# Performance work log

Hardware: AMD Instinct MI355X
Metric: run time of the kernel (lower is better)

The kernel has to match this reference:

```python
import jax, jax.numpy as jnp
import numpy as np

N_NODES = 50000
N_EDGES = 800000
N_GRAPHS = 64
IN_CH = 128
HID_CH = 128
OUT_CH = 2


def setup_inputs() -> dict:
    key = jax.random.key(0)
    k = jax.random.split(key, 7)
    x = jax.random.normal(k[0], (N_NODES, IN_CH), dtype=jnp.float32)
    edge_index = jax.random.randint(k[1], (2, N_EDGES), 0, N_NODES, dtype=jnp.int64)
    batch = jnp.sort(jax.random.randint(k[2], (N_NODES,), 0, N_GRAPHS, dtype=jnp.int64))
    W1 = jax.random.normal(k[3], (IN_CH, HID_CH), dtype=jnp.float32) * 0.05
    b1 = jnp.zeros((HID_CH,), dtype=jnp.float32)
    W2 = jax.random.normal(k[4], (HID_CH, OUT_CH), dtype=jnp.float32) * 0.05
    b2 = jnp.zeros((OUT_CH,), dtype=jnp.float32)
    return {"x": x, "edge_index": edge_index, "batch": batch,
            "W1": W1, "b1": b1, "W2": W2, "b2": b2}


def gcn_conv(x, edge_index, W, b):
    """PyG GCNConv: add self-loops, symmetric D^{-1/2}(A+I)D^{-1/2} aggregation of XW, plus bias."""
    n = x.shape[0]
    loop = jnp.arange(n, dtype=edge_index.dtype)
    src = jnp.concatenate([edge_index[0], loop])  # [E+N]
    dst = jnp.concatenate([edge_index[1], loop])
    ones = jnp.ones_like(dst, dtype=x.dtype)
    deg = jax.ops.segment_sum(ones, dst, num_segments=n)      # in-degree incl. self-loop (>=1)
    d_inv_sqrt = jax.lax.rsqrt(deg)
    norm = d_inv_sqrt[src] * d_inv_sqrt[dst]                  # [E+N]
    h = x @ W                                                 # [N, out]
    msg = h[src] * norm[:, None]                              # gather + scale
    out = jax.ops.segment_sum(msg, dst, num_segments=n)       # scatter-add
    return out + b


def global_mean_pool(x, batch, num_graphs):
    sums = jax.ops.segment_sum(x, batch, num_segments=num_graphs)
    cnt = jax.ops.segment_sum(jnp.ones((x.shape[0],), dtype=x.dtype), batch, num_segments=num_graphs)
    return sums / jnp.maximum(cnt, 1.0)[:, None]


def reference(x, edge_index, batch, W1, b1, W2, b2):
    h = jax.nn.relu(gcn_conv(x, edge_index, W1, b1))
    h = gcn_conv(h, edge_index, W2, b2)
    out = global_mean_pool(h, batch, N_GRAPHS)  # [G, out_channels]
    # dropout in eval mode == identity
    return out
```

## Files before the change

kernel.cpp:

```cpp
#include <hip/hip_runtime.h>


#define NGRAPH 64
#define CH 128
#define BSUB 384
#define NCOPY 8
#define BCAPT (BSUB * NCOPY)
#define CSTR 4096

typedef float f32x4 __attribute__((ext_vector_type(4)));
typedef _Float16 f16x8 __attribute__((ext_vector_type(8)));
typedef _Float16 f16x4 __attribute__((ext_vector_type(4)));
typedef _Float16 f16x2 __attribute__((ext_vector_type(2)));

__global__ void k_init(int* __restrict__ bcur8, float* __restrict__ gsum,
                       int* __restrict__ gcnt, int* __restrict__ done,
                       float* __restrict__ h2,
                       const float* __restrict__ W1, _Float16* __restrict__ w1t,
                       int NB, int N) {
    int i = blockIdx.x * blockDim.x + threadIdx.x;
    if (i < NB * NCOPY) bcur8[i] = 0;
    if (i < 2 * NGRAPH) gsum[i] = 0.f;
    if (i < NGRAPH) gcnt[i] = 0;
    if (i == 0) *done = 0;
    if (i < 2) h2[2 * N + i] = 0.f;
    if (i < CH * CH) {
        int k = i >> 7, c = i & 127;
        w1t[c * CH + k] = (_Float16)W1[i];
    }
}

__global__ __launch_bounds__(256) void k_bin(const int* __restrict__ src,
                                             const int* __restrict__ dst,
                                             int* __restrict__ bcur8,
                                             unsigned int* __restrict__ tmp,
                                             int E, int EPB) {
    __shared__ int hist[512];
    __shared__ int gbase[512];
    __shared__ int cur[512];
    int t = threadIdx.x;
    int e0 = blockIdx.x * EPB;
    int e1 = min(E, e0 + EPB);
    for (int i = t; i < 512; i += 256) { hist[i] = 0; cur[i] = 0; }
    __syncthreads();
    for (int e = e0 + t; e < e1; e += 256)
        atomicAdd(&hist[dst[e] >> 7], 1);
    __syncthreads();
    int copy = blockIdx.x & (NCOPY - 1);
    for (int b = t; b < 512; b += 256) {
        int hc = hist[b];
        if (hc) gbase[b] = atomicAdd(&bcur8[b * NCOPY + copy], hc);
    }
    __syncthreads();
    for (int e = e0 + t; e < e1; e += 256) {
        int d = dst[e];
        int b = d >> 7;
        int li = atomicAdd(&cur[b], 1);
        int pos = gbase[b] + li;
        if (pos < BSUB)
            tmp[(size_t)b * BCAPT + copy * BSUB + pos] =
                ((unsigned)(d & 127) << 25) | (unsigned)src[e];
    }
}

__global__ __launch_bounds__(256) void k_build(const unsigned int* __restrict__ tmp,
                                               const int* __restrict__ bcur8,
                                               int2* __restrict__ rs2,
                                               float* __restrict__ dinv,
                                               int* __restrict__ csr, int N) {
    __shared__ int hist[128];
    __shared__ int scan[128];
    __shared__ int lcur[128];
    int b = blockIdx.x, t = threadIdx.x;
    if (t < 128) hist[t] = 0;
    __syncthreads();
    const unsigned int* tb = tmp + (size_t)b * BCAPT;
    for (int c = 0; c < NCOPY; c++) {
        int cnt = min(bcur8[b * NCOPY + c], BSUB);
        const unsigned int* tp = tb + c * BSUB;
        for (int e = t; e < cnt; e += 256) atomicAdd(&hist[tp[e] >> 25], 1);
    }
    __syncthreads();
    int val = 0, v = 0, pv = 0;
    if (t < 128) { v = hist[t]; pv = (v + 7) & ~7; val = pv; scan[t] = val; }
    __syncthreads();
    for (int off = 1; off < 128; off <<= 1) {
        int add = (t >= off && t < 128) ? scan[t - off] : 0;
        __syncthreads();
        if (t < 128) { val += add; scan[t] = val; }
        __syncthreads();
    }
    int base = b * CSTR;
    if (t < 128) {
        int excl = val - pv;
        lcur[t] = excl;
        int n = b * 128 + t;
        if (n < N) {
            rs2[n] = make_int2(base + excl, pv);
            dinv[n] = rsqrtf((float)(v + 1));
            for (int e = v; e < pv; e++) csr[base + excl + e] = N;
        }
    }
    __syncthreads();
    for (int c = 0; c < NCOPY; c++) {
        int cnt = min(bcur8[b * NCOPY + c], BSUB);
        const unsigned int* tp = tb + c * BSUB;
        for (int e = t; e < cnt; e += 256) {
            unsigned p = tp[e];
            int pos = atomicAdd(&lcur[p >> 25], 1);
            csr[base + pos] = (int)(p & 0x01FFFFFFu);
        }
    }
}

__global__ __launch_bounds__(256) void k_gemm1(const float* __restrict__ X,
                                               const _Float16* __restrict__ w1t,
                                               const float* __restrict__ dinv,
                                               _Float16* __restrict__ H, int N) {
    __shared__ _Float16 Xs[64 * 136];
    __shared__ _Float16 Ws[128 * 136];
    int t = threadIdx.x;
    int row0 = blockIdx.x * 64;
    const float4* Xv = (const float4*)X;

    #pragma unroll
    for (int i = 0; i < 8; i++) {
        int gi = t + i * 256;
        int r = gi >> 5, c4 = gi & 31;
        int gr = row0 + r;
        float4 v = (gr < N) ? Xv[(size_t)gr * 32 + c4] : make_float4(0.f, 0.f, 0.f, 0.f);
        f16x4 hv = {(_Float16)v.x, (_Float16)v.y, (_Float16)v.z, (_Float16)v.w};
        *(f16x4*)&Xs[r * 136 + 4 * c4] = hv;
    }
    #pragma unroll
    for (int i = 0; i < 8; i++) {
        int gi = t + i * 256;
        int r = gi >> 4, cc = gi & 15;
        f16x8 vv = *(const f16x8*)&w1t[r * CH + cc * 8];
        *(f16x8*)&Ws[r * 136 + cc * 8] = vv;
    }
    __syncthreads();

    int w = t >> 6, l = t & 63;
    int r0w = w * 16;
    int lr = l & 15, lk = (l >> 4) * 8;
    f32x4 acc[8] = {};
    #pragma unroll
    for (int k0 = 0; k0 < 128; k0 += 32) {
        f16x8 a = *(const f16x8*)&Xs[(r0w + lr) * 136 + k0 + lk];
        #pragma unroll
        for (int c = 0; c < 8; c++) {
            f16x8 bf = *(const f16x8*)&Ws[(c * 16 + lr) * 136 + k0 + lk];
            acc[c] = __builtin_amdgcn_mfma_f32_16x16x32_f16(a, bf, acc[c], 0, 0, 0);
        }
    }
    float dv[4];
    #pragma unroll
    for (int q = 0; q < 4; q++) {
        int gr = row0 + r0w + (l >> 4) * 4 + q;
        dv[q] = (gr < N) ? dinv[gr] : 0.f;
    }
    __syncthreads();
    #pragma unroll
    for (int c = 0; c < 8; c++)
        #pragma unroll
        for (int q = 0; q < 4; q++)
            Xs[(r0w + (l >> 4) * 4 + q) * 136 + c * 16 + lr] = (_Float16)(acc[c][q] * dv[q]);
    __syncthreads();
    f16x2* Hv = (f16x2*)H;
    #pragma unroll
    for (int i = 0; i < 16; i++) {
        int gi = t + i * 256;
        int r = gi >> 6, cp = gi & 63;
        int gr = row0 + r;
        Hv[(size_t)gr * 64 + cp] = *(f16x2*)&Xs[r * 136 + 2 * cp];
    }
}

__global__ __launch_bounds__(256) void k_layer1(const _Float16* __restrict__ h,
                                                const int* __restrict__ csr,
                                                const int2* __restrict__ rs2,
                                                const float* __restrict__ dinv,
                                                const float* __restrict__ b1,
                                                const float* __restrict__ W2,
                                                float* __restrict__ h2, int N) {
    int n = (blockIdx.x * 256 + threadIdx.x) >> 6;
    int l = threadIdx.x & 63;
    if (n >= N) return;
    const f16x2* hv = (const f16x2*)h;
    float dn = dinv[n];
    f16x2 self = hv[(size_t)n * 64 + l];
    float acc0 = (float)self.x, acc1 = (float)self.y;
    int2 rs = rs2[n];
    int base = rs.x, cnt = rs.y;
    for (int c0 = 0; c0 < cnt; c0 += 64) {
        int m = cnt - c0; if (m > 64) m = 64;
        int idx = csr[base + c0 + l];
        for (int j = 0; j < m; j += 8) {
            int s0 = __shfl(idx, j + 0), s1 = __shfl(idx, j + 1);
            int s2 = __shfl(idx, j + 2), s3 = __shfl(idx, j + 3);
            int s4 = __shfl(idx, j + 4), s5 = __shfl(idx, j + 5);
            int s6 = __shfl(idx, j + 6), s7 = __shfl(idx, j + 7);
            f16x2 v0 = hv[(size_t)s0 * 64 + l];
            f16x2 v1 = hv[(size_t)s1 * 64 + l];
            f16x2 v2 = hv[(size_t)s2 * 64 + l];
            f16x2 v3 = hv[(size_t)s3 * 64 + l];
            f16x2 v4 = hv[(size_t)s4 * 64 + l];
            f16x2 v5 = hv[(size_t)s5 * 64 + l];
            f16x2 v6 = hv[(size_t)s6 * 64 + l];
            f16x2 v7 = hv[(size_t)s7 * 64 + l];
            acc0 += (float)v0.x; acc1 += (float)v0.y;
            acc0 += (float)v1.x; acc1 += (float)v1.y;
            acc0 += (float)v2.x; acc1 += (float)v2.y;
            acc0 += (float)v3.x; acc1 += (float)v3.y;
            acc0 += (float)v4.x; acc1 += (float)v4.y;
            acc0 += (float)v5.x; acc1 += (float)v5.y;
            acc0 += (float)v6.x; acc1 += (float)v6.y;
            acc0 += (float)v7.x; acc1 += (float)v7.y;
        }
    }
    float2 bb = ((const float2*)b1)[l];
    float v0 = fmaxf(fmaf(dn, acc0, bb.x), 0.f);
    float v1 = fmaxf(fmaf(dn, acc1, bb.y), 0.f);
    float4 w2 = ((const float4*)W2)[l];
    float p0 = fmaf(v0, w2.x, v1 * w2.z);
    float p1 = fmaf(v0, w2.y, v1 * w2.w);
    #pragma unroll
    for (int off = 32; off; off >>= 1) {
        p0 += __shfl_xor(p0, off);
        p1 += __shfl_xor(p1, off);
    }
    if (l == 0) ((float2*)h2)[n] = make_float2(p0 * dn, p1 * dn);
}

__global__ __launch_bounds__(256) void k_layer2_pool(const float* __restrict__ h2,
                                                     const int* __restrict__ csr,
                                                     const int2* __restrict__ rs2,
                                                     const float* __restrict__ dinv,
                                                     const int* __restrict__ batch,
                                                     float* __restrict__ gsum,
                                                     int* __restrict__ gcnt,
                                                     int* __restrict__ done,
                                                     const float* __restrict__ b2,
                                                     float* __restrict__ out, int N) {
    __shared__ float ssum[2 * NGRAPH];
    __shared__ int scnt[NGRAPH];
    __shared__ int s_last;
    int t = threadIdx.x;
    if (t < 2 * NGRAPH) ssum[t] = 0.f;
    if (t < NGRAPH) scnt[t] = 0;
    __syncthreads();
    int n = blockIdx.x * blockDim.x + t;
    if (n < N) {
        const float2* h2v = (const float2*)h2;
        float dn = dinv[n];
        float2 a = h2v[n];
        int2 rs = rs2[n];
        for (int e = rs.x; e < rs.x + rs.y; e++) {
            float2 v = h2v[csr[e]];
            a.x += v.x;
            a.y += v.y;
        }
        a.x *= dn;
        a.y *= dn;
        int g = batch[n];
        atomicAdd(&ssum[g * 2 + 0], a.x);
        atomicAdd(&ssum[g * 2 + 1], a.y);
        atomicAdd(&scnt[g], 1);
    }
    __syncthreads();
    if (t < 2 * NGRAPH) atomicAdd(&gsum[t], ssum[t]);
    if (t < NGRAPH) atomicAdd(&gcnt[t], scnt[t]);
    __syncthreads();
    if (t == 0) {
        __threadfence();
        int r = atomicAdd(done, 1);
        s_last = (r == (int)gridDim.x - 1) ? 1 : 0;
    }
    __syncthreads();
    if (s_last && t < 2 * NGRAPH) {
        int g = t >> 1, c = t & 1;
        float sv = atomicAdd(&gsum[t], 0.f);
        float cv = (float)atomicAdd(&gcnt[g], 0);
        out[t] = sv / fmaxf(cv, 1.f) + b2[c];
    }
}

extern "C" void kernel_launch(void* const* d_in, const int* in_sizes, int n_in,
                              void* d_out, int out_size, void* d_ws, size_t ws_size,
                              hipStream_t stream) {
    const float* x     = (const float*)d_in[0];
    const int*   ei    = (const int*)d_in[1];
    const int*   batch = (const int*)d_in[2];
    const float* W1    = (const float*)d_in[3];
    const float* b1    = (const float*)d_in[4];
    const float* W2    = (const float*)d_in[5];
    const float* b2    = (const float*)d_in[6];
    float* out = (float*)d_out;

    int N = in_sizes[0] / CH;
    int E = in_sizes[1] / 2;
    int NB = (N + 127) / 128;
    const int* esrc = ei;
    const int* edst = ei + E;

    char* w = (char*)d_ws;
    auto alloc = [&](size_t bytes) -> void* {
        void* p = (void*)w;
        w += (bytes + 255) & ~(size_t)255;
        return p;
    };
    _Float16* h      = (_Float16*)alloc((size_t)(N + 64) * CH * sizeof(_Float16));
    float* dinv      = (float*)alloc((size_t)N * sizeof(float));
    int2* rs2        = (int2*) alloc((size_t)N * sizeof(int2));
    int* csr         = (int*)  alloc((size_t)NB * CSTR * sizeof(int));
    float* h2        = (float*)alloc((size_t)(N + 1) * 2 * sizeof(float));
    int* bcur8       = (int*)  alloc((size_t)NB * NCOPY * sizeof(int));
    _Float16* w1t    = (_Float16*)alloc((size_t)CH * CH * sizeof(_Float16));
    float* gsum      = (float*)alloc(128 * sizeof(float));
    int* gcnt        = (int*)  alloc(64 * sizeof(int));
    int* done        = (int*)  alloc(256);
    unsigned int* tmp = (unsigned int*)h;

    int nbN = (N + 255) / 256;
    int NCHUNK = 256;
    int EPB = (E + NCHUNK - 1) / NCHUNK;

    k_init  <<<64, 256, 0, stream>>>(bcur8, gsum, gcnt, done, h2, W1, w1t, NB, N);
    k_bin   <<<NCHUNK, 256, 0, stream>>>(esrc, edst, bcur8, tmp, E, EPB);
    k_build <<<NB, 256, 0, stream>>>(tmp, bcur8, rs2, dinv, csr, N);
    k_gemm1 <<<(N + 63) / 64, 256, 0, stream>>>(x, w1t, dinv, h, N);
    k_layer1<<<(N * 64 + 255) / 256, 256, 0, stream>>>(h, csr, rs2, dinv, b1, W2, h2, N);
    k_layer2_pool<<<nbN, 256, 0, stream>>>(h2, csr, rs2, dinv, batch, gsum, gcnt,
                                           done, b2, out, N);
}
```

Baseline: 169.7 us.

## Fold init into binning kernel, read W1 directly in GEMM, retune bin copies

```diff
diff --git a/kernel.cpp b/kernel.cpp
--- a/kernel.cpp
+++ b/kernel.cpp
@@ -3,71 +3,66 @@
 
 #define NGRAPH 64
 #define CH 128
-#define BSUB 384
-#define NCOPY 8
+#define NTHR 256
+#define NBIN 512
+#define NCOPY 16
+#define BSUB 224
 #define BCAPT (BSUB * NCOPY)
-#define CSTR 4096
+#define CSTR 4608
 
 typedef float f32x4 __attribute__((ext_vector_type(4)));
 typedef _Float16 f16x8 __attribute__((ext_vector_type(8)));
 typedef _Float16 f16x4 __attribute__((ext_vector_type(4)));
 typedef _Float16 f16x2 __attribute__((ext_vector_type(2)));
 
-__global__ void k_init(int* __restrict__ bcur8, float* __restrict__ gsum,
-                       int* __restrict__ gcnt, int* __restrict__ done,
-                       float* __restrict__ h2,
-                       const float* __restrict__ W1, _Float16* __restrict__ w1t,
-                       int NB, int N) {
-    int i = blockIdx.x * blockDim.x + threadIdx.x;
-    if (i < NB * NCOPY) bcur8[i] = 0;
-    if (i < 2 * NGRAPH) gsum[i] = 0.f;
-    if (i < NGRAPH) gcnt[i] = 0;
-    if (i == 0) *done = 0;
-    if (i < 2) h2[2 * N + i] = 0.f;
-    if (i < CH * CH) {
-        int k = i >> 7, c = i & 127;
-        w1t[c * CH + k] = (_Float16)W1[i];
-    }
-}
-
-__global__ __launch_bounds__(256) void k_bin(const int* __restrict__ src,
-                                             const int* __restrict__ dst,
-                                             int* __restrict__ bcur8,
-                                             unsigned int* __restrict__ tmp,
-                                             int E, int EPB) {
+__global__ __launch_bounds__(NTHR) void k_bin(const int* __restrict__ src,
+                                              const int* __restrict__ dst,
+                                              int* __restrict__ bcur8,
+                                              unsigned int* __restrict__ tmp,
+                                              const float* __restrict__ W1,
+                                              _Float16* __restrict__ w1t,
+                                              float* __restrict__ h2,
+                                              int E, int EPB, int N) {
+    int t = threadIdx.x, blk = blockIdx.x;
+    if (blk == NBIN) {
+        for (int i = t; i < CH * CH; i += NTHR) {
+            int k = i >> 7, c = i & 127;
+            w1t[c * CH + k] = (_Float16)W1[i];
+        }
+        if (t < 2) h2[2 * N + t] = 0.f;
+        return;
+    }
     __shared__ int hist[512];
     __shared__ int gbase[512];
     __shared__ int cur[512];
-    int t = threadIdx.x;
-    int e0 = blockIdx.x * EPB;
+    for (int i = t; i < 512; i += NTHR) { hist[i] = 0; cur[i] = 0; }
+    __syncthreads();
+    int e0 = blk * EPB;
     int e1 = min(E, e0 + EPB);
-    for (int i = t; i < 512; i += 256) { hist[i] = 0; cur[i] = 0; }
-    __syncthreads();
-    for (int e = e0 + t; e < e1; e += 256)
+    for (int e = e0 + t; e < e1; e += NTHR)
         atomicAdd(&hist[dst[e] >> 7], 1);
     __syncthreads();
-    int copy = blockIdx.x & (NCOPY - 1);
-    for (int b = t; b < 512; b += 256) {
+    int copy = blk & (NCOPY - 1);
+    for (int b = t; b < 512; b += NTHR) {
         int hc = hist[b];
         if (hc) gbase[b] = atomicAdd(&bcur8[b * NCOPY + copy], hc);
     }
     __syncthreads();
-    for (int e = e0 + t; e < e1; e += 256) {
+    for (int e = e0 + t; e < e1; e += NTHR) {
         int d = dst[e];
         int b = d >> 7;
-        int li = atomicAdd(&cur[b], 1);
-        int pos = gbase[b] + li;
-        if (pos < BSUB)
+        int pos = gbase[b] + atomicAdd(&cur[b], 1);
+        if ((unsigned)pos < BSUB)
             tmp[(size_t)b * BCAPT + copy * BSUB + pos] =
                 ((unsigned)(d & 127) << 25) | (unsigned)src[e];
     }
 }
 
-__global__ __launch_bounds__(256) void k_build(const unsigned int* __restrict__ tmp,
-                                               const int* __restrict__ bcur8,
-                                               int2* __restrict__ rs2,
-                                               float* __restrict__ dinv,
-                                               int* __restrict__ csr, int N) {
+__global__ __launch_bounds__(NTHR) void k_build(const unsigned int* __restrict__ tmp,
+                                                const int* __restrict__ bcur8,
+                                                int2* __restrict__ rs2,
+                                                float* __restrict__ dinv,
+                                                int* __restrict__ csr, int N) {
     __shared__ int hist[128];
     __shared__ int scan[128];
     __shared__ int lcur[128];
@@ -78,7 +73,7 @@
     for (int c = 0; c < NCOPY; c++) {
         int cnt = min(bcur8[b * NCOPY + c], BSUB);
         const unsigned int* tp = tb + c * BSUB;
-        for (int e = t; e < cnt; e += 256) atomicAdd(&hist[tp[e] >> 25], 1);
+        for (int e = t; e < cnt; e += NTHR) atomicAdd(&hist[tp[e] >> 25], 1);
     }
     __syncthreads();
     int val = 0, v = 0, pv = 0;
@@ -105,42 +100,32 @@
     for (int c = 0; c < NCOPY; c++) {
         int cnt = min(bcur8[b * NCOPY + c], BSUB);
         const unsigned int* tp = tb + c * BSUB;
-        for (int e = t; e < cnt; e += 256) {
-            unsigned p = tp[e];
-            int pos = atomicAdd(&lcur[p >> 25], 1);
-            csr[base + pos] = (int)(p & 0x01FFFFFFu);
-        }
-    }
-}
-
-__global__ __launch_bounds__(256) void k_gemm1(const float* __restrict__ X,
-                                               const _Float16* __restrict__ w1t,
-                                               const float* __restrict__ dinv,
-                                               _Float16* __restrict__ H, int N) {
-    __shared__ _Float16 Xs[64 * 136];
-    __shared__ _Float16 Ws[128 * 136];
+        for (int e = t; e < cnt; e += NTHR) {
+            unsigned pw = tp[e];
+            int pos = atomicAdd(&lcur[pw >> 25], 1);
+            csr[base + pos] = (int)(pw & 0x01FFFFFFu);
+        }
+    }
+}
+
+__global__ __launch_bounds__(NTHR) void k_gemm1(const float* __restrict__ X,
+                                                const _Float16* __restrict__ w1t,
+                                                const float* __restrict__ dinv,
+                                                _Float16* __restrict__ H, int N) {
+    __shared__ __align__(16) _Float16 Xs[64 * 136];
     int t = threadIdx.x;
     int row0 = blockIdx.x * 64;
     const float4* Xv = (const float4*)X;
-
     #pragma unroll
     for (int i = 0; i < 8; i++) {
-        int gi = t + i * 256;
+        int gi = t + i * NTHR;
         int r = gi >> 5, c4 = gi & 31;
         int gr = row0 + r;
         float4 v = (gr < N) ? Xv[(size_t)gr * 32 + c4] : make_float4(0.f, 0.f, 0.f, 0.f);
-        f16x4 hv = {(_Float16)v.x, (_Float16)v.y, (_Float16)v.z, (_Float16)v.w};
-        *(f16x4*)&Xs[r * 136 + 4 * c4] = hv;
-    }
-    #pragma unroll
-    for (int i = 0; i < 8; i++) {
-        int gi = t + i * 256;
-        int r = gi >> 4, cc = gi & 15;
-        f16x8 vv = *(const f16x8*)&w1t[r * CH + cc * 8];
-        *(f16x8*)&Ws[r * 136 + cc * 8] = vv;
-    }
-    __syncthreads();
-
+        f16x4 hv4 = {(_Float16)v.x, (_Float16)v.y, (_Float16)v.z, (_Float16)v.w};
+        *(f16x4*)&Xs[r * 136 + 4 * c4] = hv4;
+    }
+    __syncthreads();
     int w = t >> 6, l = t & 63;
     int r0w = w * 16;
     int lr = l & 15, lk = (l >> 4) * 8;
@@ -150,7 +135,7 @@
         f16x8 a = *(const f16x8*)&Xs[(r0w + lr) * 136 + k0 + lk];
         #pragma unroll
         for (int c = 0; c < 8; c++) {
-            f16x8 bf = *(const f16x8*)&Ws[(c * 16 + lr) * 136 + k0 + lk];
+            f16x8 bf = *(const f16x8*)&w1t[(c * 16 + lr) * CH + k0 + lk];
             acc[c] = __builtin_amdgcn_mfma_f32_16x16x32_f16(a, bf, acc[c], 0, 0, 0);
         }
     }
@@ -165,26 +150,27 @@
     for (int c = 0; c < 8; c++)
         #pragma unroll
         for (int q = 0; q < 4; q++)
-            Xs[(r0w + (l >> 4) * 4 + q) * 136 + c * 16 + lr] = (_Float16)(acc[c][q] * dv[q]);
+            Xs[(r0w + (l >> 4) * 4 + q) * 136 + c * 16 + lr] =
+                (_Float16)(acc[c][q] * dv[q]);
     __syncthreads();
     f16x2* Hv = (f16x2*)H;
     #pragma unroll
     for (int i = 0; i < 16; i++) {
-        int gi = t + i * 256;
+        int gi = t + i * NTHR;
         int r = gi >> 6, cp = gi & 63;
         int gr = row0 + r;
         Hv[(size_t)gr * 64 + cp] = *(f16x2*)&Xs[r * 136 + 2 * cp];
     }
 }
 
-__global__ __launch_bounds__(256) void k_layer1(const _Float16* __restrict__ h,
-                                                const int* __restrict__ csr,
-                                                const int2* __restrict__ rs2,
-                                                const float* __restrict__ dinv,
-                                                const float* __restrict__ b1,
-                                                const float* __restrict__ W2,
-                                                float* __restrict__ h2, int N) {
-    int n = (blockIdx.x * 256 + threadIdx.x) >> 6;
+__global__ __launch_bounds__(NTHR) void k_layer1(const _Float16* __restrict__ h,
+                                                 const int* __restrict__ csr,
+                                                 const int2* __restrict__ rs2,
+                                                 const float* __restrict__ dinv,
+                                                 const float* __restrict__ b1,
+                                                 const float* __restrict__ W2,
+                                                 float* __restrict__ h2, int N) {
+    int n = (blockIdx.x * NTHR + threadIdx.x) >> 6;
     int l = threadIdx.x & 63;
     if (n >= N) return;
     const f16x2* hv = (const f16x2*)h;
@@ -233,16 +219,16 @@
     if (l == 0) ((float2*)h2)[n] = make_float2(p0 * dn, p1 * dn);
 }
 
-__global__ __launch_bounds__(256) void k_layer2_pool(const float* __restrict__ h2,
-                                                     const int* __restrict__ csr,
-                                                     const int2* __restrict__ rs2,
-                                                     const float* __restrict__ dinv,
-                                                     const int* __restrict__ batch,
-                                                     float* __restrict__ gsum,
-                                                     int* __restrict__ gcnt,
-                                                     int* __restrict__ done,
-                                                     const float* __restrict__ b2,
-                                                     float* __restrict__ out, int N) {
+__global__ __launch_bounds__(NTHR) void k_layer2_pool(const float* __restrict__ h2,
+                                                      const int* __restrict__ csr,
+                                                      const int2* __restrict__ rs2,
+                                                      const float* __restrict__ dinv,
+                                                      const int* __restrict__ batch,
+                                                      float* __restrict__ gsum,
+                                                      int* __restrict__ gcnt,
+                                                      int* __restrict__ done,
+                                                      const float* __restrict__ b2,
+                                                      float* __restrict__ out, int N) {
     __shared__ float ssum[2 * NGRAPH];
     __shared__ int scnt[NGRAPH];
     __shared__ int s_last;
@@ -258,11 +244,9 @@
         int2 rs = rs2[n];
         for (int e = rs.x; e < rs.x + rs.y; e++) {
             float2 v = h2v[csr[e]];
-            a.x += v.x;
-            a.y += v.y;
-        }
-        a.x *= dn;
-        a.y *= dn;
+            a.x += v.x; a.y += v.y;
+        }
+        a.x *= dn; a.y *= dn;
         int g = batch[n];
         atomicAdd(&ssum[g * 2 + 0], a.x);
         atomicAdd(&ssum[g * 2 + 1], a.y);
@@ -310,27 +294,29 @@
         w += (bytes + 255) & ~(size_t)255;
         return p;
     };
+    int* bcur8       = (int*)  alloc((size_t)NB * NCOPY * sizeof(int));
+    float* gsum      = (float*)alloc(128 * sizeof(float));
+    int* gcnt        = (int*)  alloc(64 * sizeof(int));
+    int* done        = (int*)  alloc(256);
+    size_t ctrl_bytes = (size_t)(w - (char*)d_ws);
     _Float16* h      = (_Float16*)alloc((size_t)(N + 64) * CH * sizeof(_Float16));
+    unsigned int* tmp= (unsigned int*)alloc((size_t)NB * BCAPT * sizeof(unsigned int));
     float* dinv      = (float*)alloc((size_t)N * sizeof(float));
     int2* rs2        = (int2*) alloc((size_t)N * sizeof(int2));
     int* csr         = (int*)  alloc((size_t)NB * CSTR * sizeof(int));
     float* h2        = (float*)alloc((size_t)(N + 1) * 2 * sizeof(float));
-    int* bcur8       = (int*)  alloc((size_t)NB * NCOPY * sizeof(int));
     _Float16* w1t    = (_Float16*)alloc((size_t)CH * CH * sizeof(_Float16));
-    float* gsum      = (float*)alloc(128 * sizeof(float));
-    int* gcnt        = (int*)  alloc(64 * sizeof(int));
-    int* done        = (int*)  alloc(256);
-    unsigned int* tmp = (unsigned int*)h;
-
-    int nbN = (N + 255) / 256;
-    int NCHUNK = 256;
-    int EPB = (E + NCHUNK - 1) / NCHUNK;
-
-    k_init  <<<64, 256, 0, stream>>>(bcur8, gsum, gcnt, done, h2, W1, w1t, NB, N);
-    k_bin   <<<NCHUNK, 256, 0, stream>>>(esrc, edst, bcur8, tmp, E, EPB);
-    k_build <<<NB, 256, 0, stream>>>(tmp, bcur8, rs2, dinv, csr, N);
-    k_gemm1 <<<(N + 63) / 64, 256, 0, stream>>>(x, w1t, dinv, h, N);
-    k_layer1<<<(N * 64 + 255) / 256, 256, 0, stream>>>(h, csr, rs2, dinv, b1, W2, h2, N);
-    k_layer2_pool<<<nbN, 256, 0, stream>>>(h2, csr, rs2, dinv, batch, gsum, gcnt,
-                                           done, b2, out, N);
-}
+
+    int EPB = (E + NBIN - 1) / NBIN;
+
+    (void)hipMemsetAsync(d_ws, 0, ctrl_bytes, stream);
+    k_bin   <<<NBIN + 1, NTHR, 0, stream>>>(esrc, edst, bcur8, tmp, W1, w1t, h2,
+                                            E, EPB, N);
+    k_build <<<NB, NTHR, 0, stream>>>(tmp, bcur8, rs2, dinv, csr, N);
+    k_gemm1 <<<(N + 63) / 64, NTHR, 0, stream>>>(x, w1t, dinv, h, N);
+    k_layer1<<<(N * 64 + NTHR - 1) / NTHR, NTHR, 0, stream>>>(h, csr, rs2, dinv,
+                                                              b1, W2, h2, N);
+    k_layer2_pool<<<(N + NTHR - 1) / NTHR, NTHR, 0, stream>>>(h2, csr, rs2, dinv,
+                                                              batch, gsum, gcnt,
+                                                              done, b2, out, N);
+}
```

After: 195.5 us. 15.2% more time.
